# Kernel tuning notes

Hardware: AMD Instinct MI355X
Metric: run time of the kernel (lower is better)

## Reference

```python
import jax, jax.numpy as jnp
import numpy as np

HEADS = 8
GROUP_SIZE = 256
DIM = 512
QK_DIM = 512
M_GLOBAL = 64


def setup_inputs() -> dict:
    key = jax.random.key(0)
    ks = jax.random.split(key, 9)
    B, N = 2, 16384
    normed_x = jax.random.normal(ks[0], (B, N, DIM), dtype=jnp.float32)
    # idx_last must be a per-batch permutation of [0, N): gather reorders tokens,
    # the final scatter puts them back.
    perm = jnp.stack([jax.random.permutation(jax.random.fold_in(ks[1], b), N) for b in range(B)])
    idx_last = perm[..., None].astype(jnp.int32)  # [B, N, 1]
    dq = QK_DIM // HEADS
    dv = DIM // HEADS
    k_global = jax.random.normal(ks[2], (HEADS, M_GLOBAL, dq), dtype=jnp.float32)
    v_global = jax.random.normal(ks[3], (HEADS, M_GLOBAL, dv), dtype=jnp.float32)
    s = 0.02
    Wq = jax.random.normal(ks[4], (DIM, QK_DIM), dtype=jnp.float32) * s
    Wk = jax.random.normal(ks[5], (DIM, QK_DIM), dtype=jnp.float32) * s
    Wv = jax.random.normal(ks[6], (DIM, DIM), dtype=jnp.float32) * s
    Wproj = jax.random.normal(ks[7], (DIM, DIM), dtype=jnp.float32) * s
    return {"normed_x": normed_x, "idx_last": idx_last, "k_global": k_global,
            "v_global": v_global, "Wq": Wq, "Wk": Wk, "Wv": Wv, "Wproj": Wproj}


def _iasa_forward(normed_x, idx_last, k_global, v_global, Wq, Wk, Wv, Wproj):
    B, N, dim = normed_x.shape
    H = HEADS
    gs = min(N, GROUP_SIZE)
    ng = -(-N // gs)
    pad_n = ng * gs - N
    q = normed_x @ Wq  # [B, N, qk]
    k = normed_x @ Wk  # [B, N, qk]
    v = normed_x @ Wv  # [B, N, dim]
    # gather-reorder tokens
    q = jnp.take_along_axis(q, jnp.broadcast_to(idx_last, q.shape), axis=1)
    k = jnp.take_along_axis(k, jnp.broadcast_to(idx_last, k.shape), axis=1)
    v = jnp.take_along_axis(v, jnp.broadcast_to(idx_last, v.shape), axis=1)
    # pad queries with flipped tail to [B, ng*gs, qk]
    pq = jnp.concatenate([q, q[:, N - pad_n:N][:, ::-1]], axis=1)
    # pad k/v with flipped last (pad_n+gs) tokens -> length (ng+1)*gs
    pk = jnp.concatenate([k, k[:, N - pad_n - gs:N][:, ::-1]], axis=1)
    pv = jnp.concatenate([v, v[:, N - pad_n - gs:N][:, ::-1]], axis=1)
    dq = pq.shape[-1] // H
    dv = dim // H
    # queries: [B, ng, H, gs, dq]
    qg = pq.reshape(B, ng, gs, H, dq).transpose(0, 1, 3, 2, 4)
    # overlapping windows of size 2*gs, stride gs (unfold equivalent)
    kgrp = pk.reshape(B, ng + 1, gs, H, dq)
    vgrp = pv.reshape(B, ng + 1, gs, H, dv)
    kwin = jnp.concatenate([kgrp[:, :-1], kgrp[:, 1:]], axis=2).transpose(0, 1, 3, 2, 4)  # [B,ng,H,2gs,dq]
    vwin = jnp.concatenate([vgrp[:, :-1], vgrp[:, 1:]], axis=2).transpose(0, 1, 3, 2, 4)  # [B,ng,H,2gs,dv]
    scale = 1.0 / jnp.sqrt(jnp.asarray(dq, dtype=qg.dtype))
    # local attention
    s1 = jnp.einsum('bghqd,bghkd->bghqk', qg, kwin) * scale
    out1 = jnp.einsum('bghqk,bghkd->bghqd', jax.nn.softmax(s1, axis=-1), vwin)
    # global attention (k_global/v_global shared across batch and groups)
    s2 = jnp.einsum('bghqd,hmd->bghqm', qg, k_global) * scale
    out2 = jnp.einsum('bghqm,hmd->bghqd', jax.nn.softmax(s2, axis=-1), v_global)
    out = (out1 + out2).transpose(0, 1, 3, 2, 4).reshape(B, ng * gs, H * dv)[:, :N]
    # scatter back (inverse of the gather, since idx_last is a permutation)
    idxo = jnp.broadcast_to(idx_last, out.shape)
    bi = jnp.arange(B)[:, None, None]
    ci = jnp.arange(H * dv)[None, None, :]
    out = out.at[bi, idxo, ci].set(out)
    return out @ Wproj


def reference(normed_x, idx_last, k_global, v_global, Wq, Wk, Wv, Wproj):
    return _iasa_forward(normed_x, idx_last, k_global, v_global, Wq, Wk, Wv, Wproj)
```

## Files before the change

kernel.cpp:

```cpp
#include <hip/hip_runtime.h>
#include <hip/hip_bf16.h>

#define B_   2
#define N_   16384
#define H_   8
#define GS_  256
#define NG_  64

typedef unsigned short u16;
typedef __attribute__((ext_vector_type(8))) short bf16x8;
typedef __attribute__((ext_vector_type(4))) float f32x4;
typedef __attribute__((ext_vector_type(8))) unsigned short us8;
typedef __attribute__((ext_vector_type(4))) unsigned short us4;
typedef __attribute__((ext_vector_type(4))) unsigned int u32x4;

__device__ __forceinline__ u16 f2b(float f){
  union { float f; unsigned u; } v; v.f = f;
  unsigned r = v.u + 0x7fffu + ((v.u >> 16) & 1u);
  return (u16)(r >> 16);
}

__device__ __forceinline__ u16 f2bh(float f){
  __hip_bfloat16 h = __float2bfloat16(f);
  u16 u; __builtin_memcpy(&u, &h, 2);
  return u;
}

__device__ __forceinline__ void gload16(const void* g, const void* lds){
  __builtin_amdgcn_global_load_lds(
      (const __attribute__((address_space(1))) void*)g,
      (__attribute__((address_space(3))) void*)lds, 16, 0, 0);
}

__device__ __forceinline__ bf16x8 lds_read8(const u16* base, int row, int coloff){
  int byte = (row*128 + coloff) ^ ((row & 7) << 4);
  return *(const bf16x8*)((const char*)base + byte);
}

__device__ __forceinline__ void stout(float* p, float v){ *p = v; }
__device__ __forceinline__ void stout(u16* p, float v){ *p = f2b(v); }

__global__ void cvt_f32_bf16(const float4* __restrict__ in, us4* __restrict__ out, int n4){
  int i = blockIdx.x * 256 + threadIdx.x;
  if (i < n4){
    float4 v = in[i];
    us4 o;
    o[0] = f2b(v.x); o[1] = f2b(v.y); o[2] = f2b(v.z); o[3] = f2b(v.w);
    out[i] = o;
  }
}

__global__ void cvt_w_t(const float* __restrict__ W0, const float* __restrict__ W1,
                        const float* __restrict__ W2, const float* __restrict__ W3,
                        u16* __restrict__ T0, u16* __restrict__ T1,
                        u16* __restrict__ T2, u16* __restrict__ T3)
{
  int z = blockIdx.z;
  const float* W = (z==0)?W0:((z==1)?W1:((z==2)?W2:W3));
  u16* T = (z==0)?T0:((z==1)?T1:((z==2)?T2:T3));
  __shared__ float tile[16][17];
  int tx = threadIdx.x & 15, ty = threadIdx.x >> 4;
  int k0 = blockIdx.x*16, n0 = blockIdx.y*16;
  tile[ty][tx] = W[(k0+ty)*512 + n0 + tx];
  __syncthreads();
  T[(n0+ty)*512 + k0 + tx] = f2b(tile[tx][ty]);
}

template<typename OUT_T, bool MULTI, bool GATHA, bool SCATC>
__global__ __launch_bounds__(256, 2) void gemm_bf16k(
    const u16* __restrict__ A,
    const u16* __restrict__ Wt0, const u16* __restrict__ Wt1, const u16* __restrict__ Wt2,
    const int* __restrict__ perm,
    OUT_T* __restrict__ C, int ldc)
{
  __shared__ u16 Al[128*64];
  __shared__ u16 Bl[128*64];
  const int tid = threadIdx.x;
  const int l = tid & 63, w = tid >> 6;
  const int lr = l & 15, lg = l >> 4;
  const int bm = blockIdx.x, bn = blockIdx.y;
  const int wr = (w >> 1) * 64, wc = (w & 1) * 64;

  const u16* Wt; int ocolb; float qsc;
  if (MULTI){
    int wsel = bn >> 2;
    Wt = (wsel == 0) ? Wt0 : ((wsel == 1) ? Wt1 : Wt2);
    ocolb = (bn & 3) * 128;
    qsc = (wsel == 0) ? 0.125f : 1.0f;
  } else { Wt = Wt0; ocolb = bn * 128; qsc = 1.0f; }

  int arows[4];
#pragma unroll
  for (int i = 0; i < 4; ++i){
    int r = bm*128 + i*32 + (tid >> 3);
    arows[i] = GATHA ? ((r & ~(N_-1)) + perm[r]) : r;
  }

  f32x4 acc[4][4];
#pragma unroll
  for (int m = 0; m < 4; ++m)
#pragma unroll
    for (int n = 0; n < 4; ++n) acc[m][n] = (f32x4){0.f,0.f,0.f,0.f};

  const int c8 = tid & 7;
  for (int kk = 0; kk < 512; kk += 64){
#pragma unroll
    for (int i = 0; i < 4; ++i){
      int o = i*4096 + tid*16;
      int brow = o >> 7;
      gload16(A  + (size_t)arows[i]*512 + kk + c8*8, (const char*)Al + i*4096 + w*1024);
      gload16(Wt + (size_t)(ocolb + brow)*512 + kk + c8*8, (const char*)Bl + i*4096 + w*1024);
    }
    __syncthreads();
#pragma unroll
    for (int ks = 0; ks < 2; ++ks){
      bf16x8 af[4], bfv[4];
#pragma unroll
      for (int m = 0; m < 4; ++m) af[m]  = *(const bf16x8*)&Al[(wr + m*16 + lr)*64 + ks*32 + lg*8];
#pragma unroll
      for (int n = 0; n < 4; ++n) bfv[n] = *(const bf16x8*)&Bl[(wc + n*16 + lr)*64 + ks*32 + lg*8];
#pragma unroll
      for (int m = 0; m < 4; ++m)
#pragma unroll
        for (int n = 0; n < 4; ++n)
          acc[m][n] = __builtin_amdgcn_mfma_f32_16x16x32_bf16(af[m], bfv[n], acc[m][n], 0, 0, 0);
    }
    __syncthreads();
  }
#pragma unroll
  for (int m = 0; m < 4; ++m)
#pragma unroll
    for (int n = 0; n < 4; ++n)
#pragma unroll
      for (int j = 0; j < 4; ++j){
        int row = bm*128 + wr + m*16 + lg*4 + j;
        int col = bn*128 + wc + n*16 + lr;
        size_t orow = SCATC ? (size_t)((row & ~(N_-1)) + perm[row]) : (size_t)row;
        stout(&C[orow*ldc + col], acc[m][n][j] * qsc);
      }
}

#define COMPUTE_CHUNK(KBUF, VBUF, ACC, LAC) do { \
  f32x4 s_[4][4]; \
  _Pragma("unroll") \
  for (int m_ = 0; m_ < 4; ++m_){ _Pragma("unroll") for (int n_ = 0; n_ < 4; ++n_) s_[m_][n_] = (f32x4){0.f,0.f,0.f,0.f}; } \
  _Pragma("unroll") \
  for (int ks_ = 0; ks_ < 2; ++ks_){ \
    bf16x8 kf_[4]; \
    _Pragma("unroll") for (int n_ = 0; n_ < 4; ++n_) kf_[n_] = lds_read8((KBUF), n_*16 + lr, ks_*64 + lg*16); \
    _Pragma("unroll") for (int m_ = 0; m_ < 4; ++m_){ \
      _Pragma("unroll") for (int n_ = 0; n_ < 4; ++n_) \
        s_[m_][n_] = __builtin_amdgcn_mfma_f32_16x16x32_bf16(qf[m_][ks_], kf_[n_], s_[m_][n_], 0, 0, 0); } } \
  _Pragma("unroll") \
  for (int m_ = 0; m_ < 4; ++m_){ _Pragma("unroll") for (int j_ = 0; j_ < 4; ++j_){ \
      float rs_ = 0.f; \
      _Pragma("unroll") for (int n_ = 0; n_ < 4; ++n_){ float p_ = __expf(s_[m_][n_][j_]); s_[m_][n_][j_] = p_; rs_ += p_; } \
      (LAC)[m_][j_] += rs_; } } \
  _Pragma("unroll") \
  for (int mh_ = 0; mh_ < 2; ++mh_){ \
    _Pragma("unroll") for (int m2_ = 0; m2_ < 2; ++m2_){ \
      _Pragma("unroll") for (int n_ = 0; n_ < 4; ++n_){ \
        _Pragma("unroll") for (int j_ = 0; j_ < 4; ++j_){ \
          int row_ = m2_*16 + lg*4 + j_, col_ = n_*16 + lr; \
          int byte_ = (row_*128 + col_*2) ^ ((row_ & 7) << 4); \
          *(u16*)((char*)Pw + byte_) = f2bh(s_[mh_*2+m2_][n_][j_]); } } } \
    _Pragma("unroll") for (int ks_ = 0; ks_ < 2; ++ks_){ \
      bf16x8 pa_[2], vb_[4]; \
      _Pragma("unroll") for (int m2_ = 0; m2_ < 2; ++m2_) pa_[m2_] = lds_read8(Pw, m2_*16 + lr, ks_*64 + lg*16); \
      _Pragma("unroll") for (int n_ = 0; n_ < 4; ++n_) vb_[n_] = lds_read8((VBUF), n_*16 + lr, ks_*64 + lg*16); \
      _Pragma("unroll") for (int m2_ = 0; m2_ < 2; ++m2_){ \
        _Pragma("unroll") for (int n_ = 0; n_ < 4; ++n_) \
          (ACC)[mh_*2+m2_][n_] = __builtin_amdgcn_mfma_f32_16x16x32_bf16(pa_[m2_], vb_[n_], (ACC)[mh_*2+m2_][n_], 0, 0, 0); } } \
  } \
} while(0)

#define LOADKV(c) do { int c_ = (c); \
  if (c_ < 8){ \
    int p0k_ = g*GS_ + c_*64 + krow_; \
    int p1k_ = p0k_ + 32; \
    int rk0_ = (p0k_ < N_) ? p0k_ : (2*N_ - 1 - p0k_); \
    int rk1_ = (p1k_ < N_) ? p1k_ : (2*N_ - 1 - p1k_); \
    kr0 = *(const us8*)(qkv + (size_t)(b*N_ + rk0_)*1536 + 512 + h*64 + kc8_*8); \
    kr1 = *(const us8*)(qkv + (size_t)(b*N_ + rk1_)*1536 + 512 + h*64 + kc8_*8); \
    int p0v_ = g*GS_ + c_*64 + 2*pair; \
    int p1v_ = p0v_ + 1; \
    int rv0_ = (p0v_ < N_) ? p0v_ : (2*N_ - 1 - p0v_); \
    int rv1_ = (p1v_ < N_) ? p1v_ : (2*N_ - 1 - p1v_); \
    vr0 = *(const us8*)(qkv + (size_t)(b*N_ + rv0_)*1536 + 1024 + h*64 + dvb*8); \
    vr1 = *(const us8*)(qkv + (size_t)(b*N_ + rv1_)*1536 + 1024 + h*64 + dvb*8); \
  } else { \
    kr0 = *(const us8*)(kgb + (size_t)(h*64 + krow_)*64 + kc8_*8); \
    kr1 = *(const us8*)(kgb + (size_t)(h*64 + 32 + krow_)*64 + kc8_*8); \
    vr0 = *(const us8*)(vgb + (size_t)(h*64 + 2*pair)*64 + dvb*8); \
    vr1 = *(const us8*)(vgb + (size_t)(h*64 + 2*pair + 1)*64 + dvb*8); \
  } } while(0)

#define WRITEKV() do { \
  { int r0_ = krow_, r1_ = 32 + krow_; \
    *(us8*)((char*)Kb + ((r0_*128 + kc8_*16) ^ ((r0_ & 7) << 4))) = kr0; \
    *(us8*)((char*)Kb + ((r1_*128 + kc8_*16) ^ ((r1_ & 7) << 4))) = kr1; } \
  _Pragma("unroll") \
  for (int j_ = 0; j_ < 8; ++j_){ \
    int r_ = dvb*8 + j_; \
    int byte_ = (r_*128 + pair*4) ^ ((r_ & 7) << 4); \
    *(unsigned*)((char*)Vb + byte_) = (unsigned)vr0[j_] | ((unsigned)vr1[j_] << 16); } \
} while(0)

__global__ __launch_bounds__(256, 2) void attn_kernel(
    const u16* __restrict__ qkv,
    const u16* __restrict__ kgb,
    const u16* __restrict__ vgb,
    u16* __restrict__ outp)
{
  __shared__ u16 Pl[4][32*64];
  __shared__ u16 Kb[64*64];
  __shared__ u16 Vb[64*64];

  const int tid = threadIdx.x;
  const int l = tid & 63, w = tid >> 6;
  const int lr = l & 15, lg = l >> 4;
  const int pair = tid & 31, dvb = tid >> 5;
  const int krow_ = tid >> 3, kc8_ = tid & 7;

  const int g = blockIdx.x, h = blockIdx.y, b = blockIdx.z;

  bf16x8 qf[4][2];
#pragma unroll
  for (int m = 0; m < 4; ++m){
    int grow = g*GS_ + w*64 + m*16 + lr;
    const u16* qrow = qkv + (size_t)(b*N_ + grow)*1536 + h*64;
#pragma unroll
    for (int ks = 0; ks < 2; ++ks)
      qf[m][ks] = *(const bf16x8*)(qrow + ks*32 + lg*8);
  }

  u16* Pw = Pl[w];

  us8 kr0, kr1, vr0, vr1;
  LOADKV(0);
  WRITEKV();
  __syncthreads();

  f32x4 oacc[4][4];
  float lrun[4][4];
#pragma unroll
  for (int m = 0; m < 4; ++m)
#pragma unroll
    for (int n = 0; n < 4; ++n) oacc[m][n] = (f32x4){0.f,0.f,0.f,0.f};
#pragma unroll
  for (int m = 0; m < 4; ++m)
#pragma unroll
    for (int j = 0; j < 4; ++j) lrun[m][j] = 0.f;

  for (int c = 0; c < 8; ++c){
    LOADKV(c + 1);
    COMPUTE_CHUNK(Kb, Vb, oacc, lrun);
    __syncthreads();
    WRITEKV();
    __syncthreads();
  }

#pragma unroll
  for (int m = 0; m < 4; ++m)
#pragma unroll
    for (int j = 0; j < 4; ++j){
      float s1 = lrun[m][j];
      s1 += __shfl_xor(s1, 1); s1 += __shfl_xor(s1, 2);
      s1 += __shfl_xor(s1, 4); s1 += __shfl_xor(s1, 8);
      float i1 = 1.f / s1;
#pragma unroll
      for (int n = 0; n < 4; ++n) oacc[m][n][j] *= i1;
    }

  {
    f32x4 s_[4][4];
#pragma unroll
    for (int m_ = 0; m_ < 4; ++m_)
#pragma unroll
      for (int n_ = 0; n_ < 4; ++n_) s_[m_][n_] = (f32x4){0.f,0.f,0.f,0.f};
#pragma unroll
    for (int ks_ = 0; ks_ < 2; ++ks_){
      bf16x8 kf_[4];
#pragma unroll
      for (int n_ = 0; n_ < 4; ++n_) kf_[n_] = lds_read8(Kb, n_*16 + lr, ks_*64 + lg*16);
#pragma unroll
      for (int m_ = 0; m_ < 4; ++m_)
#pragma unroll
        for (int n_ = 0; n_ < 4; ++n_)
          s_[m_][n_] = __builtin_amdgcn_mfma_f32_16x16x32_bf16(qf[m_][ks_], kf_[n_], s_[m_][n_], 0, 0, 0);
    }
#pragma unroll
    for (int m_ = 0; m_ < 4; ++m_)
#pragma unroll
      for (int j_ = 0; j_ < 4; ++j_){
        float rs_ = 0.f;
#pragma unroll
        for (int n_ = 0; n_ < 4; ++n_){ float p_ = __expf(s_[m_][n_][j_]); s_[m_][n_][j_] = p_; rs_ += p_; }
        rs_ += __shfl_xor(rs_, 1); rs_ += __shfl_xor(rs_, 2);
        rs_ += __shfl_xor(rs_, 4); rs_ += __shfl_xor(rs_, 8);
        float iv_ = 1.f / rs_;
#pragma unroll
        for (int n_ = 0; n_ < 4; ++n_) s_[m_][n_][j_] *= iv_;
      }
#pragma unroll
    for (int mh_ = 0; mh_ < 2; ++mh_){
#pragma unroll
      for (int m2_ = 0; m2_ < 2; ++m2_){
#pragma unroll
        for (int n_ = 0; n_ < 4; ++n_){
#pragma unroll
          for (int j_ = 0; j_ < 4; ++j_){
            int row_ = m2_*16 + lg*4 + j_, col_ = n_*16 + lr;
            int byte_ = (row_*128 + col_*2) ^ ((row_ & 7) << 4);
            *(u16*)((char*)Pw + byte_) = f2bh(s_[mh_*2+m2_][n_][j_]);
          }
        }
      }
#pragma unroll
      for (int ks_ = 0; ks_ < 2; ++ks_){
        bf16x8 pa_[2], vb_[4];
#pragma unroll
        for (int m2_ = 0; m2_ < 2; ++m2_) pa_[m2_] = lds_read8(Pw, m2_*16 + lr, ks_*64 + lg*16);
#pragma unroll
        for (int n_ = 0; n_ < 4; ++n_) vb_[n_] = lds_read8(Vb, n_*16 + lr, ks_*64 + lg*16);
#pragma unroll
        for (int m2_ = 0; m2_ < 2; ++m2_)
#pragma unroll
          for (int n_ = 0; n_ < 4; ++n_)
            oacc[mh_*2+m2_][n_] = __builtin_amdgcn_mfma_f32_16x16x32_bf16(pa_[m2_], vb_[n_], oacc[mh_*2+m2_][n_], 0, 0, 0);
      }
    }
  }

#pragma unroll
  for (int mh = 0; mh < 2; ++mh){
#pragma unroll
    for (int m2 = 0; m2 < 2; ++m2)
#pragma unroll
      for (int n = 0; n < 4; ++n)
#pragma unroll
        for (int j = 0; j < 4; ++j){
          int row = m2*16 + lg*4 + j, col = n*16 + lr;
          int byte = (row*128 + col*2) ^ ((row & 7) << 4);
          *(u16*)((char*)Pw + byte) = f2bh(oacc[mh*2+m2][n][j]);
        }
    __builtin_amdgcn_s_waitcnt(0);
#pragma unroll
    for (int i4 = 0; i4 < 4; ++i4){
      int o = i4*1024 + l*16;
      int row = o >> 7, c8 = (o & 127) >> 4;
      int addr = o ^ ((row & 7) << 4);
      u32x4 d = *(const u32x4*)((const char*)Pw + addr);
      int orow = g*GS_ + w*64 + mh*32 + row;
      *(u32x4*)(outp + (size_t)(b*N_ + orow)*512 + h*64 + c8*8) = d;
    }
  }
}

extern "C" void kernel_launch(void* const* d_in, const int* in_sizes, int n_in,
                              void* d_out, int out_size, void* d_ws, size_t ws_size,
                              hipStream_t stream)
{
  const float* x  = (const float*)d_in[0];
  const int*  idx = (const int*)d_in[1];
  const float* kg = (const float*)d_in[2];
  const float* vg = (const float*)d_in[3];
  const float* Wq = (const float*)d_in[4];
  const float* Wk = (const float*)d_in[5];
  const float* Wv = (const float*)d_in[6];
  const float* Wp = (const float*)d_in[7];
  float* out = (float*)d_out;

  char* ws = (char*)d_ws;
  u16* Xb   = (u16*)ws;
  u16* qkv  = (u16*)(ws + 33554432);
  u16* Wqt  = (u16*)(ws + 134217728);
  u16* Wkt  = (u16*)(ws + 134217728 + 524288);
  u16* Wvt  = (u16*)(ws + 134217728 + 2*524288);
  u16* Wpt  = (u16*)(ws + 134217728 + 3*524288);
  u16* kgb  = (u16*)(ws + 134217728 + 4*524288);
  u16* vgb  = (u16*)(ws + 134217728 + 4*524288 + 65536);
  u16* attn_o = Xb;

  cvt_f32_bf16<<<16384, 256, 0, stream>>>((const float4*)x, (us4*)Xb, 16777216/4);
  cvt_f32_bf16<<<32, 256, 0, stream>>>((const float4*)kg, (us4*)kgb, 32768/4);
  cvt_f32_bf16<<<32, 256, 0, stream>>>((const float4*)vg, (us4*)vgb, 32768/4);
  cvt_w_t<<<dim3(32,32,4), 256, 0, stream>>>(Wq, Wk, Wv, Wp, Wqt, Wkt, Wvt, Wpt);
  gemm_bf16k<u16, true, true, false><<<dim3(256,12), 256, 0, stream>>>(Xb, Wqt, Wkt, Wvt, idx, qkv, 1536);
  attn_kernel<<<dim3(64,8,2), 256, 0, stream>>>(qkv, kgb, vgb, attn_o);
  gemm_bf16k<float, false, false, true><<<dim3(256,4), 256, 0, stream>>>(attn_o, Wpt, Wpt, Wpt, idx, out, 512);
}
```

Baseline: 220.5 us.

## Fuse fp32-to-bf16 input conversion into QKV GEMM, use exp2 softmax, restructure P·V

Drops the separate pass that converted the whole input activation tensor to bf16. The QKV GEMM now reads fp32 rows directly and converts them while staging them into LDS, using synchronous loads instead of the direct global-to-LDS path. The Q scale is folded with log2(e) so the softmax can use exp2f instead of __expf. The attention P·V stage is reorganized into two 64-key halves with a smaller swizzled P buffer, writing P to LDS immediately after exponentiation. This removes a full read and write of the activation tensor and some exp cost, but it doubles the A-operand global traffic inside the GEMM and stalls on register-staged loads.

```diff
diff --git a/kernel.cpp b/kernel.cpp
--- a/kernel.cpp
+++ b/kernel.cpp
@@ -66,9 +66,9 @@
   T[(n0+ty)*512 + k0 + tx] = f2b(tile[tx][ty]);
 }
 
-template<typename OUT_T, bool MULTI, bool GATHA, bool SCATC>
+template<typename OUT_T, bool MULTI, bool GATHA, bool SCATC, bool AF32>
 __global__ __launch_bounds__(256, 2) void gemm_bf16k(
-    const u16* __restrict__ A,
+    const void* __restrict__ Araw,
     const u16* __restrict__ Wt0, const u16* __restrict__ Wt1, const u16* __restrict__ Wt2,
     const int* __restrict__ perm,
     OUT_T* __restrict__ C, int ldc)
@@ -86,7 +86,7 @@
     int wsel = bn >> 2;
     Wt = (wsel == 0) ? Wt0 : ((wsel == 1) ? Wt1 : Wt2);
     ocolb = (bn & 3) * 128;
-    qsc = (wsel == 0) ? 0.125f : 1.0f;
+    qsc = (wsel == 0) ? 0.18033688f : 1.0f;
   } else { Wt = Wt0; ocolb = bn * 128; qsc = 1.0f; }
 
   int arows[4];
@@ -106,9 +106,20 @@
   for (int kk = 0; kk < 512; kk += 64){
 #pragma unroll
     for (int i = 0; i < 4; ++i){
-      int o = i*4096 + tid*16;
-      int brow = o >> 7;
-      gload16(A  + (size_t)arows[i]*512 + kk + c8*8, (const char*)Al + i*4096 + w*1024);
+      if (AF32){
+        const float* As = (const float*)Araw + (size_t)arows[i]*512 + kk + c8*8;
+        float4 f0 = *(const float4*)As;
+        float4 f1 = *(const float4*)(As + 4);
+        us8 o;
+        o[0]=f2b(f0.x); o[1]=f2b(f0.y); o[2]=f2b(f0.z); o[3]=f2b(f0.w);
+        o[4]=f2b(f1.x); o[5]=f2b(f1.y); o[6]=f2b(f1.z); o[7]=f2b(f1.w);
+        *(us8*)((char*)Al + i*4096 + tid*16) = o;
+      } else {
+        gload16((const u16*)Araw + (size_t)arows[i]*512 + kk + c8*8,
+                (const char*)Al + i*4096 + w*1024);
+      }
+      int o2 = i*4096 + tid*16;
+      int brow = o2 >> 7;
       gload16(Wt + (size_t)(ocolb + brow)*512 + kk + c8*8, (const char*)Bl + i*4096 + w*1024);
     }
     __syncthreads();
@@ -140,37 +151,37 @@
       }
 }
 
+#define PBYTE(row_, col_) ((((row_)*64) + (col_)*2) ^ (((row_) & 12) << 2))
+
 #define COMPUTE_CHUNK(KBUF, VBUF, ACC, LAC) do { \
-  f32x4 s_[4][4]; \
   _Pragma("unroll") \
-  for (int m_ = 0; m_ < 4; ++m_){ _Pragma("unroll") for (int n_ = 0; n_ < 4; ++n_) s_[m_][n_] = (f32x4){0.f,0.f,0.f,0.f}; } \
-  _Pragma("unroll") \
-  for (int ks_ = 0; ks_ < 2; ++ks_){ \
-    bf16x8 kf_[4]; \
-    _Pragma("unroll") for (int n_ = 0; n_ < 4; ++n_) kf_[n_] = lds_read8((KBUF), n_*16 + lr, ks_*64 + lg*16); \
-    _Pragma("unroll") for (int m_ = 0; m_ < 4; ++m_){ \
-      _Pragma("unroll") for (int n_ = 0; n_ < 4; ++n_) \
-        s_[m_][n_] = __builtin_amdgcn_mfma_f32_16x16x32_bf16(qf[m_][ks_], kf_[n_], s_[m_][n_], 0, 0, 0); } } \
-  _Pragma("unroll") \
-  for (int m_ = 0; m_ < 4; ++m_){ _Pragma("unroll") for (int j_ = 0; j_ < 4; ++j_){ \
-      float rs_ = 0.f; \
-      _Pragma("unroll") for (int n_ = 0; n_ < 4; ++n_){ float p_ = __expf(s_[m_][n_][j_]); s_[m_][n_][j_] = p_; rs_ += p_; } \
-      (LAC)[m_][j_] += rs_; } } \
-  _Pragma("unroll") \
-  for (int mh_ = 0; mh_ < 2; ++mh_){ \
-    _Pragma("unroll") for (int m2_ = 0; m2_ < 2; ++m2_){ \
+  for (int kh_ = 0; kh_ < 2; ++kh_){ \
+    f32x4 s_[4][2]; \
+    _Pragma("unroll") \
+    for (int m_ = 0; m_ < 4; ++m_){ _Pragma("unroll") for (int n_ = 0; n_ < 2; ++n_) s_[m_][n_] = (f32x4){0.f,0.f,0.f,0.f}; } \
+    _Pragma("unroll") \
+    for (int ks_ = 0; ks_ < 2; ++ks_){ \
+      bf16x8 kf_[2]; \
+      _Pragma("unroll") for (int n_ = 0; n_ < 2; ++n_) kf_[n_] = lds_read8((KBUF), (kh_*2+n_)*16 + lr, ks_*64 + lg*16); \
+      _Pragma("unroll") for (int m_ = 0; m_ < 4; ++m_){ \
+        _Pragma("unroll") for (int n_ = 0; n_ < 2; ++n_) \
+          s_[m_][n_] = __builtin_amdgcn_mfma_f32_16x16x32_bf16(qf[m_][ks_], kf_[n_], s_[m_][n_], 0, 0, 0); } } \
+    _Pragma("unroll") \
+    for (int m_ = 0; m_ < 4; ++m_){ _Pragma("unroll") for (int j_ = 0; j_ < 4; ++j_){ \
+        float rs_ = 0.f; \
+        int row_ = m_*16 + lg*4 + j_; \
+        _Pragma("unroll") for (int n_ = 0; n_ < 2; ++n_){ \
+          float p_ = exp2f(s_[m_][n_][j_]); rs_ += p_; \
+          *(u16*)((char*)Pw + PBYTE(row_, n_*16 + lr)) = f2bh(p_); } \
+        (LAC)[m_][j_] += rs_; } } \
+    _Pragma("unroll") \
+    for (int m_ = 0; m_ < 4; ++m_){ \
+      bf16x8 pa_; \
+      { int prow_ = m_*16 + lr; \
+        pa_ = *(const bf16x8*)((const char*)Pw + ((((prow_)*64) + lg*16) ^ (((prow_) & 12) << 2))); } \
       _Pragma("unroll") for (int n_ = 0; n_ < 4; ++n_){ \
-        _Pragma("unroll") for (int j_ = 0; j_ < 4; ++j_){ \
-          int row_ = m2_*16 + lg*4 + j_, col_ = n_*16 + lr; \
-          int byte_ = (row_*128 + col_*2) ^ ((row_ & 7) << 4); \
-          *(u16*)((char*)Pw + byte_) = f2bh(s_[mh_*2+m2_][n_][j_]); } } } \
-    _Pragma("unroll") for (int ks_ = 0; ks_ < 2; ++ks_){ \
-      bf16x8 pa_[2], vb_[4]; \
-      _Pragma("unroll") for (int m2_ = 0; m2_ < 2; ++m2_) pa_[m2_] = lds_read8(Pw, m2_*16 + lr, ks_*64 + lg*16); \
-      _Pragma("unroll") for (int n_ = 0; n_ < 4; ++n_) vb_[n_] = lds_read8((VBUF), n_*16 + lr, ks_*64 + lg*16); \
-      _Pragma("unroll") for (int m2_ = 0; m2_ < 2; ++m2_){ \
-        _Pragma("unroll") for (int n_ = 0; n_ < 4; ++n_) \
-          (ACC)[mh_*2+m2_][n_] = __builtin_amdgcn_mfma_f32_16x16x32_bf16(pa_[m2_], vb_[n_], (ACC)[mh_*2+m2_][n_], 0, 0, 0); } } \
+        bf16x8 vb_ = lds_read8((VBUF), n_*16 + lr, kh_*64 + lg*16); \
+        (ACC)[m_][n_] = __builtin_amdgcn_mfma_f32_16x16x32_bf16(pa_, vb_, (ACC)[m_][n_], 0, 0, 0); } } \
   } \
 } while(0)
 
@@ -295,7 +306,7 @@
       for (int j_ = 0; j_ < 4; ++j_){
         float rs_ = 0.f;
 #pragma unroll
-        for (int n_ = 0; n_ < 4; ++n_){ float p_ = __expf(s_[m_][n_][j_]); s_[m_][n_][j_] = p_; rs_ += p_; }
+        for (int n_ = 0; n_ < 4; ++n_){ float p_ = exp2f(s_[m_][n_][j_]); s_[m_][n_][j_] = p_; rs_ += p_; }
         rs_ += __shfl_xor(rs_, 1); rs_ += __shfl_xor(rs_, 2);
         rs_ += __shfl_xor(rs_, 4); rs_ += __shfl_xor(rs_, 8);
         float iv_ = 1.f / rs_;
@@ -303,31 +314,26 @@
         for (int n_ = 0; n_ < 4; ++n_) s_[m_][n_][j_] *= iv_;
       }
 #pragma unroll
-    for (int mh_ = 0; mh_ < 2; ++mh_){
-#pragma unroll
-      for (int m2_ = 0; m2_ < 2; ++m2_){
+    for (int kh_ = 0; kh_ < 2; ++kh_){
+#pragma unroll
+      for (int m_ = 0; m_ < 4; ++m_)
+#pragma unroll
+        for (int n_ = 0; n_ < 2; ++n_)
+#pragma unroll
+          for (int j_ = 0; j_ < 4; ++j_){
+            int row_ = m_*16 + lg*4 + j_;
+            *(u16*)((char*)Pw + PBYTE(row_, n_*16 + lr)) = f2bh(s_[m_][kh_*2+n_][j_]);
+          }
+#pragma unroll
+      for (int m_ = 0; m_ < 4; ++m_){
+        bf16x8 pa_;
+        { int prow_ = m_*16 + lr;
+          pa_ = *(const bf16x8*)((const char*)Pw + ((((prow_)*64) + lg*16) ^ (((prow_) & 12) << 2))); }
 #pragma unroll
         for (int n_ = 0; n_ < 4; ++n_){
-#pragma unroll
-          for (int j_ = 0; j_ < 4; ++j_){
-            int row_ = m2_*16 + lg*4 + j_, col_ = n_*16 + lr;
-            int byte_ = (row_*128 + col_*2) ^ ((row_ & 7) << 4);
-            *(u16*)((char*)Pw + byte_) = f2bh(s_[mh_*2+m2_][n_][j_]);
-          }
+          bf16x8 vb_ = lds_read8(Vb, n_*16 + lr, kh_*64 + lg*16);
+          oacc[m_][n_] = __builtin_amdgcn_mfma_f32_16x16x32_bf16(pa_, vb_, oacc[m_][n_], 0, 0, 0);
         }
-      }
-#pragma unroll
-      for (int ks_ = 0; ks_ < 2; ++ks_){
-        bf16x8 pa_[2], vb_[4];
-#pragma unroll
-        for (int m2_ = 0; m2_ < 2; ++m2_) pa_[m2_] = lds_read8(Pw, m2_*16 + lr, ks_*64 + lg*16);
-#pragma unroll
-        for (int n_ = 0; n_ < 4; ++n_) vb_[n_] = lds_read8(Vb, n_*16 + lr, ks_*64 + lg*16);
-#pragma unroll
-        for (int m2_ = 0; m2_ < 2; ++m2_)
-#pragma unroll
-          for (int n_ = 0; n_ < 4; ++n_)
-            oacc[mh_*2+m2_][n_] = __builtin_amdgcn_mfma_f32_16x16x32_bf16(pa_[m2_], vb_[n_], oacc[mh_*2+m2_][n_], 0, 0, 0);
       }
     }
   }
@@ -372,7 +378,7 @@
   float* out = (float*)d_out;
 
   char* ws = (char*)d_ws;
-  u16* Xb   = (u16*)ws;
+  u16* attn_o = (u16*)ws;
   u16* qkv  = (u16*)(ws + 33554432);
   u16* Wqt  = (u16*)(ws + 134217728);
   u16* Wkt  = (u16*)(ws + 134217728 + 524288);
@@ -380,13 +386,13 @@
   u16* Wpt  = (u16*)(ws + 134217728 + 3*524288);
   u16* kgb  = (u16*)(ws + 134217728 + 4*524288);
   u16* vgb  = (u16*)(ws + 134217728 + 4*524288 + 65536);
-  u16* attn_o = Xb;
-
-  cvt_f32_bf16<<<16384, 256, 0, stream>>>((const float4*)x, (us4*)Xb, 16777216/4);
+
   cvt_f32_bf16<<<32, 256, 0, stream>>>((const float4*)kg, (us4*)kgb, 32768/4);
   cvt_f32_bf16<<<32, 256, 0, stream>>>((const float4*)vg, (us4*)vgb, 32768/4);
   cvt_w_t<<<dim3(32,32,4), 256, 0, stream>>>(Wq, Wk, Wv, Wp, Wqt, Wkt, Wvt, Wpt);
-  gemm_bf16k<u16, true, true, false><<<dim3(256,12), 256, 0, stream>>>(Xb, Wqt, Wkt, Wvt, idx, qkv, 1536);
+  gemm_bf16k<u16, true, true, false, true><<<dim3(256,12), 256, 0, stream>>>(
+      x, Wqt, Wkt, Wvt, idx, qkv, 1536);
   attn_kernel<<<dim3(64,8,2), 256, 0, stream>>>(qkv, kgb, vgb, attn_o);
-  gemm_bf16k<float, false, false, true><<<dim3(256,4), 256, 0, stream>>>(attn_o, Wpt, Wpt, Wpt, idx, out, 512);
-}
+  gemm_bf16k<float, false, false, true, false><<<dim3(256,4), 256, 0, stream>>>(
+      attn_o, Wpt, Wpt, Wpt, idx, out, 512);
+}
```

Measured after the change: 277.5 us. 1.26x slower.
